# Kernel optimization log

Hardware: AMD Instinct MI355X
Metric: run time of the kernel (lower is better)

## Reference

```python
import jax, jax.numpy as jnp
import numpy as np

B, S, H = 2, 2048, 1024
NH, HD = 16, 64  # num_heads, head_dim


def setup_inputs() -> dict:
    key = jax.random.key(0)
    k1, k2, k3 = jax.random.split(key, 3)
    return {
        "hidden_states": jax.random.normal(k1, (B, S, H), dtype=jnp.float32),
        "attention_mask": jnp.zeros((B, S), dtype=jnp.float32),
        "w_qkv": jax.random.normal(k2, (3 * H, H), dtype=jnp.float32) * (1.0 / np.sqrt(H)),
        "b_qkv": jnp.zeros((3 * H,), dtype=jnp.float32),
        "w_out": jax.random.normal(k3, (H, H), dtype=jnp.float32) * (1.0 / np.sqrt(H)),
        "b_out": jnp.zeros((H,), dtype=jnp.float32),
    }


def reference(hidden_states, attention_mask, w_qkv, b_qkv, w_out, b_out):
    scale = HD ** -0.5
    qkv = hidden_states @ w_qkv.T + b_qkv          # [B,S,3H]
    qkv = qkv.reshape(B, S, 3, NH, HD)
    qkv = jnp.transpose(qkv, (2, 0, 3, 1, 4))      # [3,B,NH,S,HD]
    q, k, v = qkv[0], qkv[1], qkv[2]
    scores = jnp.einsum("bhqd,bhkd->bhqk", q, k) * scale
    # 2D additive mask broadcast to [B,1,1,S] as in torch unsqueeze path
    scores = scores + attention_mask[:, None, None, :]
    attn = jax.nn.softmax(scores, axis=-1)
    out = jnp.einsum("bhqk,bhkd->bhqd", attn, v)   # [B,NH,S,HD]
    out = jnp.transpose(out, (0, 2, 1, 3)).reshape(B, S, H)
    return out @ w_out.T + b_out
```

## Files before the change

kernel.cpp:

```cpp
#include <hip/hip_runtime.h>
#include <stdint.h>

typedef short bfrag __attribute__((ext_vector_type(8)));
typedef float f32x4 __attribute__((ext_vector_type(4)));
typedef uint  uint4v __attribute__((ext_vector_type(4)));
typedef uint  uint2v __attribute__((ext_vector_type(2)));

#define LOG2E 1.4426950408889634f
#define SWZ(row) ((((row) & 3) | (((row) >> 1) & 4)) << 4)

__device__ __forceinline__ ushort f2bf(float x){
  union { float f; uint32_t u; } c; c.f = x;
  uint32_t r = (c.u + 0x7fffu + ((c.u >> 16) & 1u)) >> 16;
  return (ushort)r;
}

__device__ __forceinline__ uint32_t cvt_pk_bf16(float lo, float hi){
  uint32_t r;
  asm("v_cvt_pk_bf16_f32 %0, %1, %2" : "=v"(r) : "v"(lo), "v"(hi));
  return r;
}

__device__ __forceinline__ float redq_max(float x){
  x = fmaxf(x, __shfl_xor(x, 16));
  x = fmaxf(x, __shfl_xor(x, 32));
  return x;
}
__device__ __forceinline__ float redq_sum(float x){
  x += __shfl_xor(x, 16);
  x += __shfl_xor(x, 32);
  return x;
}

__device__ __forceinline__ void load_lds16(const void* g, void* l){
  __builtin_amdgcn_global_load_lds((const __attribute__((address_space(1))) void*)g,
                                   (__attribute__((address_space(3))) void*)l,
                                   16, 0, 0);
}

__global__ void cast_all(const float* __restrict__ hs, const float* __restrict__ wqkv,
                         const float* __restrict__ wout, const float* __restrict__ mask,
                         ushort* __restrict__ out, float* __restrict__ mask2){
  const int i = blockIdx.x * blockDim.x + threadIdx.x;
  if (i < 2097152){
    float4 f;
    if (i < 1048576)       f = ((const float4*)hs)[i];
    else if (i < 1835008)  f = ((const float4*)wqkv)[i - 1048576];
    else                   f = ((const float4*)wout)[i - 1835008];
    ushort4 u;
    u.x = f2bf(f.x); u.y = f2bf(f.y); u.z = f2bf(f.z); u.w = f2bf(f.w);
    ((ushort4*)out)[i] = u;
  } else {
    const int j = i - 2097152;
    float4 m = ((const float4*)mask)[j];
    m.x *= LOG2E; m.y *= LOG2E; m.z *= LOG2E; m.w *= LOG2E;
    ((float4*)mask2)[j] = m;
  }
}

template<int EPI>
__global__ __launch_bounds__(256)
void gemm_bt(const ushort* __restrict__ A, const ushort* __restrict__ B,
             const float* __restrict__ bias,
             ushort* __restrict__ dq, ushort* __restrict__ dk, ushort* __restrict__ dvt,
             float* __restrict__ dout,
             int M, int N, int K)
{
  __shared__ ushort Alds[2][128*32];
  __shared__ ushort Blds[2][128*32];
  const int t = threadIdx.x;
  const int w = t >> 6, l = t & 63;
  const int lr = l & 15, lg = l >> 4;
  const int m0 = blockIdx.x * 128, n0 = blockIdx.y * 128;
  const int wm = (w >> 1) * 64, wn = (w & 1) * 64;

  f32x4 acc[4][4] = {};

  auto stage = [&](int buf, int kt){
#pragma unroll
    for (int i = 0; i < 2; i++){
      const int row = i*64 + w*16 + (l >> 2);
      const int ce  = (l & 3) * 8;
      load_lds16(A + (size_t)(m0 + row) * K + kt*32 + ce, &Alds[buf][(i*64 + w*16) * 32]);
      load_lds16(B + (size_t)(n0 + row) * K + kt*32 + ce, &Blds[buf][(i*64 + w*16) * 32]);
    }
  };

  const int nk = K >> 5;
  int cur = 0;
  stage(0, 0);
  __syncthreads();
  for (int kt = 0; kt < nk; kt++){
    if (kt + 1 < nk) stage(cur ^ 1, kt + 1);
    bfrag af[4], bfv[4];
#pragma unroll
    for (int f = 0; f < 4; f++){
      af[f]  = *(const bfrag*)&Alds[cur][(wm + f*16 + lr) * 32 + lg * 8];
      bfv[f] = *(const bfrag*)&Blds[cur][(wn + f*16 + lr) * 32 + lg * 8];
    }
#pragma unroll
    for (int mf = 0; mf < 4; mf++)
#pragma unroll
      for (int nf = 0; nf < 4; nf++)
        acc[mf][nf] = __builtin_amdgcn_mfma_f32_16x16x32_bf16(af[mf], bfv[nf], acc[mf][nf], 0, 0, 0);
    __syncthreads();
    cur ^= 1;
  }

#pragma unroll
  for (int mf = 0; mf < 4; mf++){
#pragma unroll
    for (int nf = 0; nf < 4; nf++){
      const int col = n0 + wn + nf*16 + lr;
      const float bs = bias[col];
      if (EPI == 1){
        const int which = col >> 10;
        const int hd = col & 1023;
        const int bh = ((m0 >> 11) << 4) + (hd >> 6);
        const int s0 = (m0 + wm + mf*16 + lg*4) & 2047;
        if (which == 2){
          const float v0 = acc[mf][nf][0] + bs, v1 = acc[mf][nf][1] + bs;
          const float v2 = acc[mf][nf][2] + bs, v3 = acc[mf][nf][3] + bs;
          uint2v pv = { cvt_pk_bf16(v0, v1), cvt_pk_bf16(v2, v3) };
          *(uint2v*)(dvt + ((size_t)bh * 64 + (hd & 63)) * 2048 + s0) = pv;
        } else {
          ushort* dst = (which == 0) ? dq : dk;
#pragma unroll
          for (int r = 0; r < 4; r++)
            dst[((size_t)bh * 2048 + s0 + r) * 64 + (hd & 63)] = f2bf(acc[mf][nf][r] + bs);
        }
      } else {
#pragma unroll
        for (int r = 0; r < 4; r++){
          const int row = m0 + wm + mf*16 + lg*4 + r;
          dout[(size_t)row * N + col] = acc[mf][nf][r] + bs;
        }
      }
    }
  }
}

__global__ __launch_bounds__(256, 2)
void flash_attn(const ushort* __restrict__ q, const ushort* __restrict__ k,
                const ushort* __restrict__ vt, const float* __restrict__ mask2,
                ushort* __restrict__ ao)
{
  __shared__ ushort Klds[2][64*64];
  __shared__ ushort Vlds[2][64*64];
  const int t = threadIdx.x;
  const int w = t >> 6, l = t & 63;
  const int lr = l & 15, lg = l >> 4;
  const int bh = blockIdx.y;
  const int b = bh >> 4, h = bh & 15;
  const int q0 = blockIdx.x * 128;
  const ushort* qb  = q  + (size_t)bh * 2048 * 64;
  const ushort* kb  = k  + (size_t)bh * 2048 * 64;
  const ushort* vtb = vt + (size_t)bh * 64 * 2048;
  const float* mb = mask2 + b * 2048;

  const int srow0 = t >> 3;
  const int scol  = (t & 7) * 16;

  auto stageKV = [&](int buf, int kv0){
#pragma unroll
    for (int i = 0; i < 2; i++){
      const int row = srow0 + i*32;
      const int off = scol ^ SWZ(row);
      load_lds16((const char*)(kb + (size_t)kv0 * 64) + row*128 + off,
                 (char*)&Klds[buf][0] + i*4096 + w*1024);
      load_lds16((const char*)vtb + (size_t)row * 4096 + kv0*2 + off,
                 (char*)&Vlds[buf][0] + i*4096 + w*1024);
    }
  };

  bfrag qf[2][2];
#pragma unroll
  for (int qg = 0; qg < 2; qg++)
#pragma unroll
    for (int kf = 0; kf < 2; kf++){
      const int row = q0 + w*32 + qg*16 + lr;
      qf[qg][kf] = *(const bfrag*)(qb + (size_t)row * 64 + kf*32 + lg*8);
    }

  float mrun[2] = {-1e30f, -1e30f}, lsum[2] = {0.f, 0.f};
  f32x4 oacc[2][4] = {};

  const float SC2 = 0.125f * LOG2E;
  const int rbase = (lr >> 2) * 8 + (lr & 3);

  stageKV(0, 0);

  int cur = 0;
  for (int kv0 = 0; kv0 < 2048; kv0 += 64){
    __syncthreads();
    if (kv0 + 64 < 2048) stageKV(cur ^ 1, kv0 + 64);

    float4 mk[4];
#pragma unroll
    for (int nf = 0; nf < 4; nf++)
      mk[nf] = *(const float4*)(mb + kv0 + ((nf & 1) << 5) + (lg << 3) + ((nf >> 1) << 2));

    bfrag bk[4][2];
#pragma unroll
    for (int nf = 0; nf < 4; nf++){
      const int rho = ((nf & 1) << 5) + ((nf >> 1) << 2) + rbase;
      const int rsw = SWZ(rho);
#pragma unroll
      for (int kf = 0; kf < 2; kf++){
        const int kbyte = kf*64 + lg*16;
        bk[nf][kf] = *(const bfrag*)((const char*)&Klds[cur][0] + rho*128 + (kbyte ^ rsw));
      }
    }
    f32x4 sa[2][4] = {};
#pragma unroll
    for (int qg = 0; qg < 2; qg++)
#pragma unroll
      for (int nf = 0; nf < 4; nf++)
#pragma unroll
        for (int kf = 0; kf < 2; kf++)
          sa[qg][nf] = __builtin_amdgcn_mfma_f32_16x16x32_bf16(bk[nf][kf], qf[qg][kf], sa[qg][nf], 0, 0, 0);

    float sc[2][4][4], mx[2];
#pragma unroll
    for (int qg = 0; qg < 2; qg++){
#pragma unroll
      for (int nf = 0; nf < 4; nf++){
        sc[qg][nf][0] = fmaf(sa[qg][nf][0], SC2, mk[nf].x);
        sc[qg][nf][1] = fmaf(sa[qg][nf][1], SC2, mk[nf].y);
        sc[qg][nf][2] = fmaf(sa[qg][nf][2], SC2, mk[nf].z);
        sc[qg][nf][3] = fmaf(sa[qg][nf][3], SC2, mk[nf].w);
      }
      float m01 = fmaxf(fmaxf(sc[qg][0][0], sc[qg][0][1]), fmaxf(sc[qg][0][2], sc[qg][0][3]));
#pragma unroll
      for (int nf = 1; nf < 4; nf++)
#pragma unroll
        for (int r = 0; r < 4; r++) m01 = fmaxf(m01, sc[qg][nf][r]);
      mx[qg] = m01;
    }

    const bool grew = (mx[0] > mrun[0] + 8.f) | (mx[1] > mrun[1] + 8.f);
    if (__any(grew)){
#pragma unroll
      for (int qg = 0; qg < 2; qg++){
        const float mnew = fmaxf(mrun[qg], redq_max(mx[qg]));
        const float c = __builtin_amdgcn_exp2f(mrun[qg] - mnew);
        mrun[qg] = mnew;
        lsum[qg] *= c;
#pragma unroll
        for (int nf = 0; nf < 4; nf++) oacc[qg][nf] *= c;
      }
    }

    bfrag ap[2][2];
#pragma unroll
    for (int qg = 0; qg < 2; qg++){
      float ps = 0.f;
#pragma unroll
      for (int nf = 0; nf < 4; nf++)
#pragma unroll
        for (int r = 0; r < 4; r++){
          sc[qg][nf][r] = __builtin_amdgcn_exp2f(sc[qg][nf][r] - mrun[qg]);
          ps += sc[qg][nf][r];
        }
      lsum[qg] += ps;
#pragma unroll
      for (int kf = 0; kf < 2; kf++){
        uint4v tv = { cvt_pk_bf16(sc[qg][kf][0],   sc[qg][kf][1]),
                      cvt_pk_bf16(sc[qg][kf][2],   sc[qg][kf][3]),
                      cvt_pk_bf16(sc[qg][kf+2][0], sc[qg][kf+2][1]),
                      cvt_pk_bf16(sc[qg][kf+2][2], sc[qg][kf+2][3]) };
        ap[qg][kf] = __builtin_bit_cast(bfrag, tv);
      }
    }

    bfrag bv[4][2];
#pragma unroll
    for (int nf = 0; nf < 4; nf++)
#pragma unroll
      for (int kf = 0; kf < 2; kf++){
        const int d = nf*16 + lr;
        const int kbyte = kf*64 + lg*16;
        bv[nf][kf] = *(const bfrag*)((const char*)&Vlds[cur][0] + d*128 + (kbyte ^ SWZ(d)));
      }
#pragma unroll
    for (int qg = 0; qg < 2; qg++)
#pragma unroll
      for (int nf = 0; nf < 4; nf++)
#pragma unroll
        for (int kf = 0; kf < 2; kf++)
          oacc[qg][nf] = __builtin_amdgcn_mfma_f32_16x16x32_bf16(bv[nf][kf], ap[qg][kf], oacc[qg][nf], 0, 0, 0);

    cur ^= 1;
  }

#pragma unroll
  for (int qg = 0; qg < 2; qg++){
    const float inv = 1.f / redq_sum(lsum[qg]);
    ushort* orow = ao + (size_t)(b*2048 + q0 + w*32 + qg*16 + lr) * 1024 + h*64 + lg*4;
#pragma unroll
    for (int nf = 0; nf < 4; nf++){
      const uint32_t w01 = cvt_pk_bf16(oacc[qg][nf][0] * inv, oacc[qg][nf][1] * inv);
      const uint32_t w23 = cvt_pk_bf16(oacc[qg][nf][2] * inv, oacc[qg][nf][3] * inv);
      uint2v vv = {w01, w23};
      *(uint2v*)(orow + nf*16) = vv;
    }
  }
}

extern "C" void kernel_launch(void* const* d_in, const int* in_sizes, int n_in,
                              void* d_out, int out_size, void* d_ws, size_t ws_size,
                              hipStream_t stream)
{
  (void)in_sizes; (void)n_in; (void)out_size; (void)ws_size;
  const float* hs   = (const float*)d_in[0];
  const float* mask = (const float*)d_in[1];
  const float* wqkv = (const float*)d_in[2];
  const float* bqkv = (const float*)d_in[3];
  const float* wout = (const float*)d_in[4];
  const float* bout = (const float*)d_in[5];
  float* out = (float*)d_out;

  char* ws = (char*)d_ws;
  ushort* hs_bf = (ushort*)(ws);
  ushort* w1_bf = (ushort*)(ws + 8388608);
  ushort* w2_bf = (ushort*)(ws + 14680064);
  ushort* q_bf  = (ushort*)(ws + 16777216);
  ushort* k_bf  = (ushort*)(ws + 25165824);
  ushort* vt_bf = (ushort*)(ws + 33554432);
  ushort* ao_bf = (ushort*)(ws + 41943040);
  float*  mask2 = (float*)(ws + 50331648);

  cast_all<<<8196, 256, 0, stream>>>(hs, wqkv, wout, mask, (ushort*)ws, mask2);

  gemm_bt<1><<<dim3(32, 24), 256, 0, stream>>>(hs_bf, w1_bf, bqkv,
                                               q_bf, k_bf, vt_bf, nullptr,
                                               4096, 3072, 1024);
  flash_attn<<<dim3(16, 32), 256, 0, stream>>>(q_bf, k_bf, vt_bf, mask2, ao_bf);
  gemm_bt<2><<<dim3(32, 8), 256, 0, stream>>>(ao_bf, w2_bf, bout,
                                              nullptr, nullptr, nullptr, out,
                                              4096, 1024, 1024);
}
```

Baseline: 127.8 us.

## Split attention KV range across two blocks and merge partial softmax results

Flash attention now launches a third grid dimension that splits the 2048-key range into two halves. Each half writes a normalized bf16 partial output plus its per-row max and sum, and a new merge kernel combines them into the final attention output. The grid goes from 512 to 1024 blocks, aimed at filling more CUs on the GPU. In exchange it adds an extra kernel launch, extra global traffic for the partials, and a second bf16 rounding of the output. The workspace is reshuffled so the partials overwrite the hidden-state cast buffer, and the cast of w_out moves to a new location.

```diff
diff --git a/kernel.cpp b/kernel.cpp
--- a/kernel.cpp
+++ b/kernel.cpp
@@ -14,6 +14,10 @@
   uint32_t r = (c.u + 0x7fffu + ((c.u >> 16) & 1u)) >> 16;
   return (ushort)r;
 }
+__device__ __forceinline__ float bf2f(ushort u){
+  union { uint32_t u; float f; } c; c.u = ((uint32_t)u) << 16;
+  return c.f;
+}
 
 __device__ __forceinline__ uint32_t cvt_pk_bf16(float lo, float hi){
   uint32_t r;
@@ -40,16 +44,18 @@
 
 __global__ void cast_all(const float* __restrict__ hs, const float* __restrict__ wqkv,
                          const float* __restrict__ wout, const float* __restrict__ mask,
-                         ushort* __restrict__ out, float* __restrict__ mask2){
+                         ushort* __restrict__ out, ushort* __restrict__ w2,
+                         float* __restrict__ mask2){
   const int i = blockIdx.x * blockDim.x + threadIdx.x;
   if (i < 2097152){
     float4 f;
+    ushort4 u;
     if (i < 1048576)       f = ((const float4*)hs)[i];
     else if (i < 1835008)  f = ((const float4*)wqkv)[i - 1048576];
     else                   f = ((const float4*)wout)[i - 1835008];
-    ushort4 u;
     u.x = f2bf(f.x); u.y = f2bf(f.y); u.z = f2bf(f.z); u.w = f2bf(f.w);
-    ((ushort4*)out)[i] = u;
+    if (i < 1835008) ((ushort4*)out)[i] = u;
+    else             ((ushort4*)w2)[i - 1835008] = u;
   } else {
     const int j = i - 2097152;
     float4 m = ((const float4*)mask)[j];
@@ -143,7 +149,8 @@
 __global__ __launch_bounds__(256, 2)
 void flash_attn(const ushort* __restrict__ q, const ushort* __restrict__ k,
                 const ushort* __restrict__ vt, const float* __restrict__ mask2,
-                ushort* __restrict__ ao)
+                ushort* __restrict__ opart, float* __restrict__ mpart,
+                float* __restrict__ lpart)
 {
   __shared__ ushort Klds[2][64*64];
   __shared__ ushort Vlds[2][64*64];
@@ -151,8 +158,10 @@
   const int w = t >> 6, l = t & 63;
   const int lr = l & 15, lg = l >> 4;
   const int bh = blockIdx.y;
-  const int b = bh >> 4, h = bh & 15;
+  const int b = bh >> 4;
+  const int z = blockIdx.z;
   const int q0 = blockIdx.x * 128;
+  const int kvbase = z * 1024;
   const ushort* qb  = q  + (size_t)bh * 2048 * 64;
   const ushort* kb  = k  + (size_t)bh * 2048 * 64;
   const ushort* vtb = vt + (size_t)bh * 64 * 2048;
@@ -188,12 +197,12 @@
   const float SC2 = 0.125f * LOG2E;
   const int rbase = (lr >> 2) * 8 + (lr & 3);
 
-  stageKV(0, 0);
+  stageKV(0, kvbase);
 
   int cur = 0;
-  for (int kv0 = 0; kv0 < 2048; kv0 += 64){
+  for (int kv0 = kvbase; kv0 < kvbase + 1024; kv0 += 64){
     __syncthreads();
-    if (kv0 + 64 < 2048) stageKV(cur ^ 1, kv0 + 64);
+    if (kv0 + 64 < kvbase + 1024) stageKV(cur ^ 1, kv0 + 64);
 
     float4 mk[4];
 #pragma unroll
@@ -295,8 +304,14 @@
 
 #pragma unroll
   for (int qg = 0; qg < 2; qg++){
-    const float inv = 1.f / redq_sum(lsum[qg]);
-    ushort* orow = ao + (size_t)(b*2048 + q0 + w*32 + qg*16 + lr) * 1024 + h*64 + lg*4;
+    const int row = q0 + w*32 + qg*16 + lr;
+    const float ltot = redq_sum(lsum[qg]);
+    const float inv = 1.f / ltot;
+    if (lg == 0){
+      mpart[((size_t)z*32 + bh)*2048 + row] = mrun[qg];
+      lpart[((size_t)z*32 + bh)*2048 + row] = ltot;
+    }
+    ushort* orow = opart + (size_t)z*16777216/2 + ((size_t)bh*2048 + row)*64 + lg*4;
 #pragma unroll
     for (int nf = 0; nf < 4; nf++){
       const uint32_t w01 = cvt_pk_bf16(oacc[qg][nf][0] * inv, oacc[qg][nf][1] * inv);
@@ -305,6 +320,36 @@
       *(uint2v*)(orow + nf*16) = vv;
     }
   }
+}
+
+__global__ __launch_bounds__(256)
+void merge_halves(const ushort* __restrict__ opart, const float* __restrict__ mpart,
+                  const float* __restrict__ lpart, ushort* __restrict__ ao){
+  const int idx = blockIdx.x * 256 + threadIdx.x;
+  const int row = idx >> 7;
+  const int col0 = (idx & 127) * 8;
+  const int h = col0 >> 6;
+  const int b = row >> 11, s = row & 2047;
+  const int bh = b*16 + h;
+  const float m0 = mpart[(size_t)bh*2048 + s], m1 = mpart[(size_t)(32+bh)*2048 + s];
+  const float l0 = lpart[(size_t)bh*2048 + s], l1 = lpart[(size_t)(32+bh)*2048 + s];
+  const float m = fmaxf(m0, m1);
+  const float a0 = __builtin_amdgcn_exp2f(m0 - m) * l0;
+  const float a1 = __builtin_amdgcn_exp2f(m1 - m) * l1;
+  const float inv = 1.f / (a0 + a1);
+  const float c0 = a0 * inv, c1 = a1 * inv;
+  const size_t pix = ((size_t)bh*2048 + s)*64 + (col0 & 63);
+  bfrag f0 = *(const bfrag*)(opart + pix);
+  bfrag f1 = *(const bfrag*)(opart + 8388608 + pix);
+  uint32_t wds[4];
+#pragma unroll
+  for (int j = 0; j < 4; j++){
+    const float x0 = c0*bf2f((ushort)f0[2*j  ]) + c1*bf2f((ushort)f1[2*j  ]);
+    const float x1 = c0*bf2f((ushort)f0[2*j+1]) + c1*bf2f((ushort)f1[2*j+1]);
+    wds[j] = cvt_pk_bf16(x0, x1);
+  }
+  uint4v vv = {wds[0], wds[1], wds[2], wds[3]};
+  *(uint4v*)(ao + (size_t)row*1024 + col0) = vv;
 }
 
 extern "C" void kernel_launch(void* const* d_in, const int* in_sizes, int n_in,
@@ -323,19 +368,24 @@
   char* ws = (char*)d_ws;
   ushort* hs_bf = (ushort*)(ws);
   ushort* w1_bf = (ushort*)(ws + 8388608);
-  ushort* w2_bf = (ushort*)(ws + 14680064);
+  ushort* opart = (ushort*)(ws);
   ushort* q_bf  = (ushort*)(ws + 16777216);
   ushort* k_bf  = (ushort*)(ws + 25165824);
   ushort* vt_bf = (ushort*)(ws + 33554432);
   ushort* ao_bf = (ushort*)(ws + 41943040);
-  float*  mask2 = (float*)(ws + 50331648);
-
-  cast_all<<<8196, 256, 0, stream>>>(hs, wqkv, wout, mask, (ushort*)ws, mask2);
+  float*  mpart = (float*)(ws + 50331648);
+  float*  lpart = (float*)(ws + 50855936);
+  float*  mask2 = (float*)(ws + 51380224);
+  ushort* w2_bf = (ushort*)(ws + 51396608);
+
+  cast_all<<<8196, 256, 0, stream>>>(hs, wqkv, wout, mask, (ushort*)ws, w2_bf, mask2);
 
   gemm_bt<1><<<dim3(32, 24), 256, 0, stream>>>(hs_bf, w1_bf, bqkv,
                                                q_bf, k_bf, vt_bf, nullptr,
                                                4096, 3072, 1024);
-  flash_attn<<<dim3(16, 32), 256, 0, stream>>>(q_bf, k_bf, vt_bf, mask2, ao_bf);
+  flash_attn<<<dim3(16, 32, 2), 256, 0, stream>>>(q_bf, k_bf, vt_bf, mask2,
+                                                  opart, mpart, lpart);
+  merge_halves<<<2048, 256, 0, stream>>>(opart, mpart, lpart, ao_bf);
   gemm_bt<2><<<dim3(32, 8), 256, 0, stream>>>(ao_bf, w2_bf, bout,
                                               nullptr, nullptr, nullptr, out,
                                               4096, 1024, 1024);
```

Measured after the change: 138.7 us. +8.5%, slower.
